# Kernel tuning notes

Hardware: AMD Instinct MI355X
Metric: run time of the kernel (lower is better)

The kernel has to match this reference:

```python
import jax, jax.numpy as jnp
import numpy as np
import math

B, T, C = 2, 2048, 1024
N_HEADS = 16  # config.head_size in the original (actually number of heads)
HEAD_DIM = C // N_HEADS


def setup_inputs() -> dict:
    key = jax.random.key(0)
    k1, k2, k3 = jax.random.split(key, 3)
    s = 1.0 / math.sqrt(C)
    return {
        "x": jax.random.normal(k1, (B, T, C), dtype=jnp.float32),
        "W_attn": jax.random.normal(k2, (C, 3 * C), dtype=jnp.float32) * s,
        "b_attn": jnp.zeros((3 * C,), dtype=jnp.float32),
        "W_proj": jax.random.normal(k3, (C, C), dtype=jnp.float32) * s,
        "b_proj": jnp.zeros((C,), dtype=jnp.float32),
    }


def reference(x, W_attn, b_attn, W_proj, b_proj):
    Bsz, Tlen, Cdim = x.shape
    qkv = x @ W_attn + b_attn                      # [B,T,3C]
    q, k, v = jnp.split(qkv, 3, axis=-1)
    # [B,T,C] -> [B,H,T,D]
    def to_heads(t):
        return t.reshape(Bsz, Tlen, N_HEADS, HEAD_DIM).transpose(0, 2, 1, 3)
    q, k, v = to_heads(q), to_heads(k), to_heads(v)
    # NOTE: original multiplies by sqrt(head_dim) (faithful to source, not 1/sqrt)
    scale = jnp.asarray(math.sqrt(HEAD_DIM), dtype=x.dtype)
    att = jnp.einsum("bhqd,bhkd->bhqk", q, k) * scale
    causal = jnp.tril(jnp.ones((Tlen, Tlen), dtype=bool))
    att = jnp.where(causal[None, None, :, :], att, jnp.asarray(-jnp.inf, x.dtype))
    att = jax.nn.softmax(att, axis=-1)
    # dropout layers are identity in eval mode
    y = jnp.einsum("bhqk,bhkd->bhqd", att, v)
    y = y.transpose(0, 2, 1, 3).reshape(Bsz, Tlen, Cdim)
    return y @ W_proj + b_proj
```

## Files before the change

kernel.cpp:

```cpp
#include <hip/hip_runtime.h>
#include <hip/hip_bf16.h>


#define B_  2
#define T_  2048
#define C_  1024
#define H_  16
#define D_  64
#define M_  (B_ * T_)
#define N3_ (3 * C_)

typedef __attribute__((ext_vector_type(8))) short s16x8;
typedef __attribute__((ext_vector_type(4))) short s16x4;
typedef __attribute__((ext_vector_type(4))) float f32x4;

typedef const __attribute__((address_space(1))) unsigned int gu32_t;
typedef __attribute__((address_space(3))) unsigned int lu32_t;

#define MFMA16(a, b, c) __builtin_amdgcn_mfma_f32_16x16x32_bf16(a, b, c, 0, 0, 0)

__device__ __forceinline__ void gload_lds16(const short* g, short* l) {
    __builtin_amdgcn_global_load_lds((gu32_t*)g, (lu32_t*)l, 16, 0, 0);
}

__device__ __forceinline__ float b2f(unsigned short u) {
    return __uint_as_float(((unsigned)u) << 16);
}
__device__ __forceinline__ unsigned short f2b(float f) {
    unsigned u = __float_as_uint(f);
    return (unsigned short)((u + 0x7FFFu + ((u >> 16) & 1u)) >> 16);
}
__device__ __forceinline__ float fexp2(float x) {
#if __has_builtin(__builtin_amdgcn_exp2f)
    return __builtin_amdgcn_exp2f(x);
#else
    return exp2f(x);
#endif
}

__global__ __launch_bounds__(256) void cvt_split(
    const float* __restrict__ in, short* __restrict__ oh, short* __restrict__ ol, int n)
{
    int i = (blockIdx.x * 256 + threadIdx.x) * 8;
    if (i >= n) return;
    float4 a = *(const float4*)&in[i];
    float4 b = *(const float4*)&in[i + 4];
    float v[8] = {a.x, a.y, a.z, a.w, b.x, b.y, b.z, b.w};
    s16x8 h, l;
    #pragma unroll
    for (int j = 0; j < 8; j++) {
        unsigned short hb = f2b(v[j]);
        h[j] = (short)hb;
        l[j] = (short)f2b(v[j] - b2f(hb));
    }
    *(s16x8*)&oh[i] = h;
    *(s16x8*)&ol[i] = l;
}

__global__ __launch_bounds__(256) void cvtT_split(
    const float* __restrict__ in, short* __restrict__ oh, short* __restrict__ ol,
    int R, int Cn)
{
    __shared__ short th[64][80];
    __shared__ short tl[64][80];
    const int tid = threadIdx.x;
    const int k0 = blockIdx.y * 64;
    const int n0 = blockIdx.x * 64;
    {
        int rl = tid >> 4, cl = (tid & 15) * 4;
        #pragma unroll
        for (int i = 0; i < 4; i++) {
            int kr = rl + i * 16;
            float4 v4 = *(const float4*)&in[(size_t)(k0 + kr) * Cn + n0 + cl];
            float v[4] = {v4.x, v4.y, v4.z, v4.w};
            #pragma unroll
            for (int j = 0; j < 4; j++) {
                unsigned short hb = f2b(v[j]);
                th[cl + j][kr] = (short)hb;
                tl[cl + j][kr] = (short)f2b(v[j] - b2f(hb));
            }
        }
    }
    __syncthreads();
    {
        int ro = tid >> 2, co = (tid & 3) * 16;
        *(s16x8*)&oh[(size_t)(n0 + ro) * R + k0 + co]     = *(s16x8*)&th[ro][co];
        *(s16x8*)&oh[(size_t)(n0 + ro) * R + k0 + co + 8] = *(s16x8*)&th[ro][co + 8];
        *(s16x8*)&ol[(size_t)(n0 + ro) * R + k0 + co]     = *(s16x8*)&tl[ro][co];
        *(s16x8*)&ol[(size_t)(n0 + ro) * R + k0 + co + 8] = *(s16x8*)&tl[ro][co + 8];
    }
}

__global__ __launch_bounds__(256) void cvtT_bf16(
    const float* __restrict__ in, short* __restrict__ out, int R, int Cn)
{
    __shared__ short t[64][80];
    const int tid = threadIdx.x;
    const int k0 = blockIdx.y * 64;
    const int n0 = blockIdx.x * 64;
    {
        int rl = tid >> 4, cl = (tid & 15) * 4;
        #pragma unroll
        for (int i = 0; i < 4; i++) {
            int kr = rl + i * 16;
            float4 v = *(const float4*)&in[(size_t)(k0 + kr) * Cn + n0 + cl];
            t[cl + 0][kr] = (short)f2b(v.x);
            t[cl + 1][kr] = (short)f2b(v.y);
            t[cl + 2][kr] = (short)f2b(v.z);
            t[cl + 3][kr] = (short)f2b(v.w);
        }
    }
    __syncthreads();
    {
        int ro = tid >> 2, co = (tid & 3) * 16;
        *(s16x8*)&out[(size_t)(n0 + ro) * R + k0 + co]     = *(s16x8*)&t[ro][co];
        *(s16x8*)&out[(size_t)(n0 + ro) * R + k0 + co + 8] = *(s16x8*)&t[ro][co + 8];
    }
}

__global__ __launch_bounds__(256) void qkv_qk(
    const short* __restrict__ Ah, const short* __restrict__ Al,
    const short* __restrict__ BTh, const short* __restrict__ BTl,
    const float* __restrict__ bias,
    short* __restrict__ Qh, short* __restrict__ Ql,
    short* __restrict__ Kh, short* __restrict__ Kl)
{
    __shared__ short Ash[128 * 32], Asl[128 * 32];
    __shared__ short Bsh[128 * 32], Bsl[128 * 32];

    const int tid  = threadIdx.x;
    const int wave = tid >> 6, lane = tid & 63;
    const int wm = wave >> 1, wn = wave & 1;
    const int lm = lane & 15, lq = lane >> 4;
    const int m0 = blockIdx.y * 128, n0 = blockIdx.x * 128;
    const int gr  = (lane >> 2);
    const int gc  = (((lane & 3) ^ ((lane >> 3) & 3)) << 3);
    const int sg  = ((lq ^ ((lm >> 1) & 3)) << 3);

    f32x4 acc[4][4] = {};

    for (int k0 = 0; k0 < C_; k0 += 32) {
        __syncthreads();
        #pragma unroll
        for (int j = 0; j < 2; j++) {
            int s = wave * 2 + j;
            int row = s * 16 + gr;
            size_t ga = (size_t)(m0 + row) * C_ + k0 + gc;
            size_t gb = (size_t)(n0 + row) * C_ + k0 + gc;
            gload_lds16(&Ah[ga],  &Ash[s * 512]);
            gload_lds16(&Al[ga],  &Asl[s * 512]);
            gload_lds16(&BTh[gb], &Bsh[s * 512]);
            gload_lds16(&BTl[gb], &Bsl[s * 512]);
        }
        __syncthreads();

        s16x8 ah[4], al[4], bh[4], bl[4];
        #pragma unroll
        for (int mi = 0; mi < 4; mi++) {
            int r = wm * 64 + mi * 16 + lm;
            ah[mi] = *(const s16x8*)&Ash[r * 32 + sg];
            al[mi] = *(const s16x8*)&Asl[r * 32 + sg];
        }
        #pragma unroll
        for (int nj = 0; nj < 4; nj++) {
            int r = wn * 64 + nj * 16 + lm;
            bh[nj] = *(const s16x8*)&Bsh[r * 32 + sg];
            bl[nj] = *(const s16x8*)&Bsl[r * 32 + sg];
        }
        #pragma unroll
        for (int mi = 0; mi < 4; mi++)
            #pragma unroll
            for (int nj = 0; nj < 4; nj++) {
                acc[mi][nj] = MFMA16(ah[mi], bh[nj], acc[mi][nj]);
                acc[mi][nj] = MFMA16(ah[mi], bl[nj], acc[mi][nj]);
                acc[mi][nj] = MFMA16(al[mi], bh[nj], acc[mi][nj]);
            }
    }

    #pragma unroll
    for (int nj = 0; nj < 4; nj++) {
        int n = n0 + wn * 64 + nj * 16 + lm;
        float bv = bias[n];
        int isK = n >> 10;
        int c = n & (C_ - 1);
        int h = c >> 6, d = c & (D_ - 1);
        short* dh = isK ? Kh : Qh;
        short* dl = isK ? Kl : Ql;
        float scale = isK ? 1.0f : 11.541560327111708f;
        #pragma unroll
        for (int mi = 0; mi < 4; mi++) {
            #pragma unroll
            for (int r = 0; r < 4; r++) {
                int m  = m0 + wm * 64 + mi * 16 + lq * 4 + r;
                int bb = m >> 11, t = m & (T_ - 1);
                float v = (acc[mi][nj][r] + bv) * scale;
                size_t idx = (((size_t)bb * H_ + h) * T_ + t) * D_ + d;
                unsigned short hb = f2b(v);
                dh[idx] = (short)hb;
                dl[idx] = (short)f2b(v - b2f(hb));
            }
        }
    }
}

__global__ __launch_bounds__(256, 4) void qkv_v(
    const short* __restrict__ Ah, const short* __restrict__ BTh,
    const float* __restrict__ bias, short* __restrict__ VT)
{
    __shared__ short Ash[64 * 32];
    __shared__ short Bsh[128 * 32];

    const int tid  = threadIdx.x;
    const int wave = tid >> 6, lane = tid & 63;
    const int wm = wave >> 1, wn = wave & 1;
    const int lm = lane & 15, lq = lane >> 4;
    const int m0 = blockIdx.y * 64, n0 = blockIdx.x * 128;
    const int gr  = (lane >> 2);
    const int gc  = (((lane & 3) ^ ((lane >> 3) & 3)) << 3);
    const int sg  = ((lq ^ ((lm >> 1) & 3)) << 3);

    f32x4 acc[2][4] = {};

    for (int k0 = 0; k0 < C_; k0 += 32) {
        __syncthreads();
        {
            int rowA = wave * 16 + gr;
            gload_lds16(&Ah[(size_t)(m0 + rowA) * C_ + k0 + gc], &Ash[wave * 512]);
            #pragma unroll
            for (int j = 0; j < 2; j++) {
                int s = wave * 2 + j;
                int rowB = s * 16 + gr;
                gload_lds16(&BTh[(size_t)(n0 + rowB) * C_ + k0 + gc], &Bsh[s * 512]);
            }
        }
        __syncthreads();

        s16x8 af[2], bfr[4];
        #pragma unroll
        for (int mi = 0; mi < 2; mi++)
            af[mi] = *(const s16x8*)&Ash[(wm * 32 + mi * 16 + lm) * 32 + sg];
        #pragma unroll
        for (int nj = 0; nj < 4; nj++)
            bfr[nj] = *(const s16x8*)&Bsh[(wn * 64 + nj * 16 + lm) * 32 + sg];
        #pragma unroll
        for (int mi = 0; mi < 2; mi++)
            #pragma unroll
            for (int nj = 0; nj < 4; nj++)
                acc[mi][nj] = MFMA16(af[mi], bfr[nj], acc[mi][nj]);
    }

    #pragma unroll
    for (int nj = 0; nj < 4; nj++) {
        int n = n0 + wn * 64 + nj * 16 + lm;
        float bv = bias[n];
        int h = n >> 6, d = n & (D_ - 1);
        #pragma unroll
        for (int mi = 0; mi < 2; mi++) {
            #pragma unroll
            for (int r = 0; r < 4; r++) {
                int m  = m0 + wm * 32 + mi * 16 + lq * 4 + r;
                int bb = m >> 11, t = m & (T_ - 1);
                VT[(((size_t)bb * H_ + h) * D_ + d) * T_ + t] =
                    (short)f2b(acc[mi][nj][r] + bv);
            }
        }
    }
}

__global__ __launch_bounds__(256, 4) void proj_mfma(
    const short* __restrict__ Ah, const short* __restrict__ BTh,
    const float* __restrict__ bias, float* __restrict__ out)
{
    __shared__ short Ash[64 * 32];
    __shared__ short Bsh[128 * 32];

    const int tid  = threadIdx.x;
    const int wave = tid >> 6, lane = tid & 63;
    const int wm = wave >> 1, wn = wave & 1;
    const int lm = lane & 15, lq = lane >> 4;
    const int m0 = blockIdx.y * 64, n0 = blockIdx.x * 128;
    const int gr  = (lane >> 2);
    const int gc  = (((lane & 3) ^ ((lane >> 3) & 3)) << 3);
    const int sg  = ((lq ^ ((lm >> 1) & 3)) << 3);

    f32x4 acc[2][4] = {};

    for (int k0 = 0; k0 < C_; k0 += 32) {
        __syncthreads();
        {
            int rowA = wave * 16 + gr;
            gload_lds16(&Ah[(size_t)(m0 + rowA) * C_ + k0 + gc], &Ash[wave * 512]);
            #pragma unroll
            for (int j = 0; j < 2; j++) {
                int s = wave * 2 + j;
                int rowB = s * 16 + gr;
                gload_lds16(&BTh[(size_t)(n0 + rowB) * C_ + k0 + gc], &Bsh[s * 512]);
            }
        }
        __syncthreads();

        s16x8 af[2], bfr[4];
        #pragma unroll
        for (int mi = 0; mi < 2; mi++)
            af[mi] = *(const s16x8*)&Ash[(wm * 32 + mi * 16 + lm) * 32 + sg];
        #pragma unroll
        for (int nj = 0; nj < 4; nj++)
            bfr[nj] = *(const s16x8*)&Bsh[(wn * 64 + nj * 16 + lm) * 32 + sg];
        #pragma unroll
        for (int mi = 0; mi < 2; mi++)
            #pragma unroll
            for (int nj = 0; nj < 4; nj++)
                acc[mi][nj] = MFMA16(af[mi], bfr[nj], acc[mi][nj]);
    }

    #pragma unroll
    for (int nj = 0; nj < 4; nj++) {
        int n = n0 + wn * 64 + nj * 16 + lm;
        float bv = bias[n];
        #pragma unroll
        for (int mi = 0; mi < 2; mi++) {
            #pragma unroll
            for (int r = 0; r < 4; r++) {
                int m = m0 + wm * 32 + mi * 16 + lq * 4 + r;
                out[(size_t)m * C_ + n] = acc[mi][nj][r] + bv;
            }
        }
    }
}

__device__ __forceinline__ void online_sm(
    f32x4 S[4], float& mrow, float& lrow, f32x4 O[4], int quad)
{
    float v[16];
    #pragma unroll
    for (int t = 0; t < 4; t++)
        #pragma unroll
        for (int r = 0; r < 4; r++) v[t * 4 + r] = S[t][r];
    #pragma unroll
    for (int s = 8; s; s >>= 1)
        #pragma unroll
        for (int i = 0; i < s; i++) v[i] = fmaxf(v[i], v[i + s]);
    float rm = v[0];
    rm = fmaxf(rm, __shfl_xor(rm, 16, 64));
    rm = fmaxf(rm, __shfl_xor(rm, 32, 64));
    if (!__all(rm - mrow <= 8.f)) {
        float mnew  = fmaxf(mrow, rm);
        float alpha = fexp2(mrow - mnew);
        mrow = mnew;
        lrow *= alpha;
        float al[4];
        #pragma unroll
        for (int r = 0; r < 4; r++) al[r] = __shfl(alpha, quad * 4 + r, 64);
        #pragma unroll
        for (int t = 0; t < 4; t++)
            #pragma unroll
            for (int r = 0; r < 4; r++) O[t][r] *= al[r];
    }
    float sv[16];
    #pragma unroll
    for (int t = 0; t < 4; t++)
        #pragma unroll
        for (int r = 0; r < 4; r++) {
            float p = fexp2(S[t][r] - mrow);
            S[t][r] = p;
            sv[t * 4 + r] = p;
        }
    #pragma unroll
    for (int s = 8; s; s >>= 1)
        #pragma unroll
        for (int i = 0; i < s; i++) sv[i] += sv[i + s];
    float rs = sv[0];
    rs += __shfl_xor(rs, 16, 64);
    rs += __shfl_xor(rs, 32, 64);
    lrow += rs;
}

__global__ __launch_bounds__(256, 2) void attn_mfma(
    const short* __restrict__ Qh, const short* __restrict__ Ql,
    const short* __restrict__ Kh, const short* __restrict__ Kl,
    const short* __restrict__ VT, short* __restrict__ Yb)
{
    __shared__ short Ksh[64][64], Ksl[64][64];
    __shared__ short Vt [64][64];
    __shared__ short Ps [4][2][16][64];

    const int tid  = threadIdx.x;
    const int wave = tid >> 6, lane = tid & 63;
    const int lm   = lane & 15, quad = lane >> 4;
    const int swz  = (lm & 7) << 3;

    const int bid = blockIdx.x;
    const int xcd = bid & 7;
    const int r_  = bid >> 3;
    const int bhl = r_ & 3;
    const int u   = r_ >> 2;
    const int g_  = u >> 3, j_ = u & 7;
    const int j   = g_ ? (15 - j_) : j_;
    const int bh  = xcd * 4 + bhl;
    const int b   = bh >> 4, h = bh & (H_ - 1);
    const int qtA = j, qtB = 31 - j;
    const int q0A = qtA * 64, q0B = qtB * 64;
    const size_t base  = (size_t)bh * T_ * D_;
    const size_t vbase = (size_t)bh * D_ * T_;

    const int src = tid >> 3;
    const int sch = (tid & 7) * 8;
    const int wsw = sch ^ ((src & 7) << 3);

    s16x8 bqhA[2], bqlA[2], bqhB[2], bqlB[2];
    #pragma unroll
    for (int kc = 0; kc < 2; kc++) {
        size_t ga = base + (size_t)(q0A + wave * 16 + lm) * D_ + kc * 32 + quad * 8;
        size_t gb = base + (size_t)(q0B + wave * 16 + lm) * D_ + kc * 32 + quad * 8;
        bqhA[kc] = *(const s16x8*)&Qh[ga];
        bqlA[kc] = *(const s16x8*)&Ql[ga];
        bqhB[kc] = *(const s16x8*)&Qh[gb];
        bqlB[kc] = *(const s16x8*)&Ql[gb];
    }

    s16x8 pkh[2], pkl[2], pvt[2];
    #pragma unroll
    for (int i = 0; i < 2; i++) {
        int row = i * 32 + src;
        size_t gk = base + (size_t)row * D_ + sch;
        pkh[i] = *(const s16x8*)&Kh[gk];
        pkl[i] = *(const s16x8*)&Kl[gk];
        pvt[i] = *(const s16x8*)&VT[vbase + (size_t)row * T_ + sch];
    }

    float mA = -INFINITY, lA = 0.f;
    float mB = -INFINITY, lB = 0.f;
    f32x4 OA[4] = {}, OB[4] = {};

    for (int kt = 0; kt <= qtB; kt++) {
        __syncthreads();
        #pragma unroll
        for (int i = 0; i < 2; i++) {
            int row = i * 32 + src;
            *(s16x8*)&Ksh[row][wsw] = pkh[i];
            *(s16x8*)&Ksl[row][wsw] = pkl[i];
            *(s16x8*)&Vt [row][wsw] = pvt[i];
        }
        if (kt < qtB) {
            #pragma unroll
            for (int i = 0; i < 2; i++) {
                int row = i * 32 + src;
                size_t gk = base + (size_t)((kt + 1) * 64 + row) * D_ + sch;
                pkh[i] = *(const s16x8*)&Kh[gk];
                pkl[i] = *(const s16x8*)&Kl[gk];
                pvt[i] = *(const s16x8*)&VT[vbase + (size_t)row * T_ + (kt + 1) * 64 + sch];
            }
        }
        __syncthreads();

        const bool doA = (kt <= qtA);
        const int  qg  = wave * 16 + lm;

        f32x4 SB[4] = {}, SA[4] = {};
        if (doA) {
            #pragma unroll
            for (int t = 0; t < 4; t++)
                #pragma unroll
                for (int kc = 0; kc < 2; kc++) {
                    s16x8 kh8 = *(const s16x8*)&Ksh[t * 16 + lm][(kc * 32 + quad * 8) ^ swz];
                    s16x8 kl8 = *(const s16x8*)&Ksl[t * 16 + lm][(kc * 32 + quad * 8) ^ swz];
                    SB[t] = MFMA16(kh8, bqhB[kc], SB[t]);
                    SB[t] = MFMA16(kl8, bqhB[kc], SB[t]);
                    SB[t] = MFMA16(kh8, bqlB[kc], SB[t]);
                    SA[t] = MFMA16(kh8, bqhA[kc], SA[t]);
                    SA[t] = MFMA16(kl8, bqhA[kc], SA[t]);
                    SA[t] = MFMA16(kh8, bqlA[kc], SA[t]);
                }
        } else {
            #pragma unroll
            for (int t = 0; t < 4; t++)
                #pragma unroll
                for (int kc = 0; kc < 2; kc++) {
                    s16x8 kh8 = *(const s16x8*)&Ksh[t * 16 + lm][(kc * 32 + quad * 8) ^ swz];
                    s16x8 kl8 = *(const s16x8*)&Ksl[t * 16 + lm][(kc * 32 + quad * 8) ^ swz];
                    SB[t] = MFMA16(kh8, bqhB[kc], SB[t]);
                    SB[t] = MFMA16(kl8, bqhB[kc], SB[t]);
                    SB[t] = MFMA16(kh8, bqlB[kc], SB[t]);
                }
        }

        if (kt == qtB) {
            #pragma unroll
            for (int t = 0; t < 4; t++)
                #pragma unroll
                for (int r = 0; r < 4; r++)
                    if ((t * 16 + quad * 4 + r) > qg) SB[t][r] = -INFINITY;
        }
        if (kt == qtA) {
            #pragma unroll
            for (int t = 0; t < 4; t++)
                #pragma unroll
                for (int r = 0; r < 4; r++)
                    if ((t * 16 + quad * 4 + r) > qg) SA[t][r] = -INFINITY;
        }

        online_sm(SB, mB, lB, OB, quad);
        if (doA) online_sm(SA, mA, lA, OA, quad);

        #pragma unroll
        for (int t = 0; t < 4; t++) {
            s16x4 p;
            #pragma unroll
            for (int r = 0; r < 4; r++)
                p[r] = (short)(__float_as_uint(SB[t][r]) >> 16);
            *(s16x4*)&Ps[wave][0][lm][(t * 16 + quad * 4) ^ swz] = p;
        }
        if (doA) {
            #pragma unroll
            for (int t = 0; t < 4; t++) {
                s16x4 p;
                #pragma unroll
                for (int r = 0; r < 4; r++)
                    p[r] = (short)(__float_as_uint(SA[t][r]) >> 16);
                *(s16x4*)&Ps[wave][1][lm][(t * 16 + quad * 4) ^ swz] = p;
            }
        }

        s16x8 apB[2], apA[2];
        #pragma unroll
        for (int kc = 0; kc < 2; kc++)
            apB[kc] = *(const s16x8*)&Ps[wave][0][lm][(kc * 32 + quad * 8) ^ swz];
        if (doA) {
            #pragma unroll
            for (int kc = 0; kc < 2; kc++)
                apA[kc] = *(const s16x8*)&Ps[wave][1][lm][(kc * 32 + quad * 8) ^ swz];
            #pragma unroll
            for (int t = 0; t < 4; t++)
                #pragma unroll
                for (int kc = 0; kc < 2; kc++) {
                    s16x8 bv = *(const s16x8*)&Vt[t * 16 + lm][(kc * 32 + quad * 8) ^ swz];
                    OB[t] = MFMA16(apB[kc], bv, OB[t]);
                    OA[t] = MFMA16(apA[kc], bv, OA[t]);
                }
        } else {
            #pragma unroll
            for (int t = 0; t < 4; t++)
                #pragma unroll
                for (int kc = 0; kc < 2; kc++) {
                    s16x8 bv = *(const s16x8*)&Vt[t * 16 + lm][(kc * 32 + quad * 8) ^ swz];
                    OB[t] = MFMA16(apB[kc], bv, OB[t]);
                }
        }
    }

    float liA[4], liB[4];
    #pragma unroll
    for (int r = 0; r < 4; r++) {
        liA[r] = 1.0f / __shfl(lA, quad * 4 + r, 64);
        liB[r] = 1.0f / __shfl(lB, quad * 4 + r, 64);
    }
    #pragma unroll
    for (int t = 0; t < 4; t++)
        #pragma unroll
        for (int r = 0; r < 4; r++) {
            int d  = t * 16 + lm;
            int qa = q0A + wave * 16 + quad * 4 + r;
            int qb = q0B + wave * 16 + quad * 4 + r;
            Yb[((size_t)b * T_ + qa) * C_ + h * D_ + d] =
                (short)f2b(OA[t][r] * liA[r]);
            Yb[((size_t)b * T_ + qb) * C_ + h * D_ + d] =
                (short)f2b(OB[t][r] * liB[r]);
        }
}

extern "C" void kernel_launch(void* const* d_in, const int* in_sizes, int n_in,
                              void* d_out, int out_size, void* d_ws, size_t ws_size,
                              hipStream_t stream)
{
    const float* x      = (const float*)d_in[0];
    const float* W_attn = (const float*)d_in[1];
    const float* b_attn = (const float*)d_in[2];
    const float* W_proj = (const float*)d_in[3];
    const float* b_proj = (const float*)d_in[4];
    float* out = (float*)d_out;

    char* ws = (char*)d_ws;
    const size_t MB = 1024 * 1024;
    short* Qh   = (short*)(ws);
    short* Ql   = (short*)(ws +  8 * MB);
    short* Kh   = (short*)(ws + 16 * MB);
    short* Kl   = (short*)(ws + 24 * MB);
    short* xh   = (short*)(ws + 32 * MB);
    short* xl   = (short*)(ws + 40 * MB);
    short* WaTh = (short*)(ws + 48 * MB);
    short* WaTl = (short*)(ws + 54 * MB);
    short* WpT  = (short*)(ws + 60 * MB);
    short* VT   = (short*)(ws + 40 * MB);
    short* Yb   = (short*)(ws + 32 * MB);

    cvt_split <<<dim3(M_ * C_ / 2048), 256, 0, stream>>>(x, xh, xl, M_ * C_);
    cvtT_split<<<dim3(N3_ / 64, C_ / 64), 256, 0, stream>>>(W_attn, WaTh, WaTl, C_, N3_);
    cvtT_bf16 <<<dim3(C_ / 64, C_ / 64), 256, 0, stream>>>(W_proj, WpT, C_, C_);

    qkv_qk <<<dim3(16, 32), 256, 0, stream>>>(xh, xl, WaTh, WaTl, b_attn,
                                              Qh, Ql, Kh, Kl);
    qkv_v  <<<dim3(8, 64), 256, 0, stream>>>(xh, WaTh + (size_t)2048 * C_,
                                             b_attn + 2048, VT);
    attn_mfma<<<dim3(512), 256, 0, stream>>>(Qh, Ql, Kh, Kl, VT, Yb);
    proj_mfma<<<dim3(8, 64), 256, 0, stream>>>(Yb, WpT, b_proj, out);
}
```

Before: 241.6 us.

## Double-buffer LDS in GEMM kernels with async prefetch two stages ahead

The three GEMM kernels (qkv_qk, qkv_v, proj_mfma) now use two LDS buffers. Global-to-LDS loads are issued two k-steps ahead and gated by explicit vmcnt waits and raw s_barrier, so memory latency overlaps MFMA work. The attention kernel also swaps __syncthreads for a raw barrier plus an lgkmcnt wait. This doubles LDS use per block, which may lower occupancy. The hand-written waitcnt counts must match the number of loads issued, otherwise the pipeline can race.

```diff
diff --git a/kernel.cpp b/kernel.cpp
--- a/kernel.cpp
+++ b/kernel.cpp
@@ -118,6 +118,20 @@
     }
 }
 
+#define QK_STAGE(buf, kk) do {                                          \
+    _Pragma("unroll")                                                   \
+    for (int j = 0; j < 2; j++) {                                       \
+        int s = wave * 2 + j;                                           \
+        int row = s * 16 + gr;                                          \
+        size_t ga = (size_t)(m0 + row) * C_ + (kk) + gc;                \
+        size_t gb = (size_t)(n0 + row) * C_ + (kk) + gc;                \
+        gload_lds16(&Ah[ga],  &Ash[buf][s * 512]);                      \
+        gload_lds16(&Al[ga],  &Asl[buf][s * 512]);                      \
+        gload_lds16(&BTh[gb], &Bsh[buf][s * 512]);                      \
+        gload_lds16(&BTl[gb], &Bsl[buf][s * 512]);                      \
+    }                                                                   \
+} while (0)
+
 __global__ __launch_bounds__(256) void qkv_qk(
     const short* __restrict__ Ah, const short* __restrict__ Al,
     const short* __restrict__ BTh, const short* __restrict__ BTl,
@@ -125,8 +139,8 @@
     short* __restrict__ Qh, short* __restrict__ Ql,
     short* __restrict__ Kh, short* __restrict__ Kl)
 {
-    __shared__ short Ash[128 * 32], Asl[128 * 32];
-    __shared__ short Bsh[128 * 32], Bsl[128 * 32];
+    __shared__ short Ash[2][128 * 32], Asl[2][128 * 32];
+    __shared__ short Bsh[2][128 * 32], Bsl[2][128 * 32];
 
     const int tid  = threadIdx.x;
     const int wave = tid >> 6, lane = tid & 63;
@@ -139,33 +153,28 @@
 
     f32x4 acc[4][4] = {};
 
-    for (int k0 = 0; k0 < C_; k0 += 32) {
-        __syncthreads();
-        #pragma unroll
-        for (int j = 0; j < 2; j++) {
-            int s = wave * 2 + j;
-            int row = s * 16 + gr;
-            size_t ga = (size_t)(m0 + row) * C_ + k0 + gc;
-            size_t gb = (size_t)(n0 + row) * C_ + k0 + gc;
-            gload_lds16(&Ah[ga],  &Ash[s * 512]);
-            gload_lds16(&Al[ga],  &Asl[s * 512]);
-            gload_lds16(&BTh[gb], &Bsh[s * 512]);
-            gload_lds16(&BTl[gb], &Bsl[s * 512]);
-        }
-        __syncthreads();
+    QK_STAGE(0, 0);
+    QK_STAGE(1, 32);
+
+    for (int it = 0; it < 32; ++it) {
+        const int cur = it & 1;
+        if (it == 31) asm volatile("s_waitcnt vmcnt(0)" ::: "memory");
+        else          asm volatile("s_waitcnt vmcnt(8)" ::: "memory");
+        __builtin_amdgcn_s_barrier();
+        __builtin_amdgcn_sched_barrier(0);
 
         s16x8 ah[4], al[4], bh[4], bl[4];
         #pragma unroll
         for (int mi = 0; mi < 4; mi++) {
             int r = wm * 64 + mi * 16 + lm;
-            ah[mi] = *(const s16x8*)&Ash[r * 32 + sg];
-            al[mi] = *(const s16x8*)&Asl[r * 32 + sg];
+            ah[mi] = *(const s16x8*)&Ash[cur][r * 32 + sg];
+            al[mi] = *(const s16x8*)&Asl[cur][r * 32 + sg];
         }
         #pragma unroll
         for (int nj = 0; nj < 4; nj++) {
             int r = wn * 64 + nj * 16 + lm;
-            bh[nj] = *(const s16x8*)&Bsh[r * 32 + sg];
-            bl[nj] = *(const s16x8*)&Bsl[r * 32 + sg];
+            bh[nj] = *(const s16x8*)&Bsh[cur][r * 32 + sg];
+            bl[nj] = *(const s16x8*)&Bsl[cur][r * 32 + sg];
         }
         #pragma unroll
         for (int mi = 0; mi < 4; mi++)
@@ -175,6 +184,10 @@
                 acc[mi][nj] = MFMA16(ah[mi], bl[nj], acc[mi][nj]);
                 acc[mi][nj] = MFMA16(al[mi], bh[nj], acc[mi][nj]);
             }
+
+        __builtin_amdgcn_sched_barrier(0);
+        __builtin_amdgcn_s_barrier();
+        if (it < 30) QK_STAGE(cur, (it + 2) * 32);
     }
 
     #pragma unroll
@@ -203,12 +216,27 @@
     }
 }
 
+#define V_STAGE(buf, kk) do {                                           \
+    {                                                                   \
+        int rowA = wave * 16 + gr;                                      \
+        gload_lds16(&Ah[(size_t)(m0 + rowA) * C_ + (kk) + gc],          \
+                    &Ash[buf][wave * 512]);                             \
+        _Pragma("unroll")                                               \
+        for (int j = 0; j < 2; j++) {                                   \
+            int s = wave * 2 + j;                                       \
+            int rowB = s * 16 + gr;                                     \
+            gload_lds16(&BTh[(size_t)(n0 + rowB) * C_ + (kk) + gc],     \
+                        &Bsh[buf][s * 512]);                            \
+        }                                                               \
+    }                                                                   \
+} while (0)
+
 __global__ __launch_bounds__(256, 4) void qkv_v(
     const short* __restrict__ Ah, const short* __restrict__ BTh,
     const float* __restrict__ bias, short* __restrict__ VT)
 {
-    __shared__ short Ash[64 * 32];
-    __shared__ short Bsh[128 * 32];
+    __shared__ short Ash[2][64 * 32];
+    __shared__ short Bsh[2][128 * 32];
 
     const int tid  = threadIdx.x;
     const int wave = tid >> 6, lane = tid & 63;
@@ -221,32 +249,32 @@
 
     f32x4 acc[2][4] = {};
 
-    for (int k0 = 0; k0 < C_; k0 += 32) {
-        __syncthreads();
-        {
-            int rowA = wave * 16 + gr;
-            gload_lds16(&Ah[(size_t)(m0 + rowA) * C_ + k0 + gc], &Ash[wave * 512]);
-            #pragma unroll
-            for (int j = 0; j < 2; j++) {
-                int s = wave * 2 + j;
-                int rowB = s * 16 + gr;
-                gload_lds16(&BTh[(size_t)(n0 + rowB) * C_ + k0 + gc], &Bsh[s * 512]);
-            }
-        }
-        __syncthreads();
+    V_STAGE(0, 0);
+    V_STAGE(1, 32);
+
+    for (int it = 0; it < 32; ++it) {
+        const int cur = it & 1;
+        if (it == 31) asm volatile("s_waitcnt vmcnt(0)" ::: "memory");
+        else          asm volatile("s_waitcnt vmcnt(3)" ::: "memory");
+        __builtin_amdgcn_s_barrier();
+        __builtin_amdgcn_sched_barrier(0);
 
         s16x8 af[2], bfr[4];
         #pragma unroll
         for (int mi = 0; mi < 2; mi++)
-            af[mi] = *(const s16x8*)&Ash[(wm * 32 + mi * 16 + lm) * 32 + sg];
+            af[mi] = *(const s16x8*)&Ash[cur][(wm * 32 + mi * 16 + lm) * 32 + sg];
         #pragma unroll
         for (int nj = 0; nj < 4; nj++)
-            bfr[nj] = *(const s16x8*)&Bsh[(wn * 64 + nj * 16 + lm) * 32 + sg];
+            bfr[nj] = *(const s16x8*)&Bsh[cur][(wn * 64 + nj * 16 + lm) * 32 + sg];
         #pragma unroll
         for (int mi = 0; mi < 2; mi++)
             #pragma unroll
             for (int nj = 0; nj < 4; nj++)
                 acc[mi][nj] = MFMA16(af[mi], bfr[nj], acc[mi][nj]);
+
+        __builtin_amdgcn_sched_barrier(0);
+        __builtin_amdgcn_s_barrier();
+        if (it < 30) V_STAGE(cur, (it + 2) * 32);
     }
 
     #pragma unroll
@@ -271,8 +299,8 @@
     const short* __restrict__ Ah, const short* __restrict__ BTh,
     const float* __restrict__ bias, float* __restrict__ out)
 {
-    __shared__ short Ash[64 * 32];
-    __shared__ short Bsh[128 * 32];
+    __shared__ short Ash[2][64 * 32];
+    __shared__ short Bsh[2][128 * 32];
 
     const int tid  = threadIdx.x;
     const int wave = tid >> 6, lane = tid & 63;
@@ -285,32 +313,32 @@
 
     f32x4 acc[2][4] = {};
 
-    for (int k0 = 0; k0 < C_; k0 += 32) {
-        __syncthreads();
-        {
-            int rowA = wave * 16 + gr;
-            gload_lds16(&Ah[(size_t)(m0 + rowA) * C_ + k0 + gc], &Ash[wave * 512]);
-            #pragma unroll
-            for (int j = 0; j < 2; j++) {
-                int s = wave * 2 + j;
-                int rowB = s * 16 + gr;
-                gload_lds16(&BTh[(size_t)(n0 + rowB) * C_ + k0 + gc], &Bsh[s * 512]);
-            }
-        }
-        __syncthreads();
+    V_STAGE(0, 0);
+    V_STAGE(1, 32);
+
+    for (int it = 0; it < 32; ++it) {
+        const int cur = it & 1;
+        if (it == 31) asm volatile("s_waitcnt vmcnt(0)" ::: "memory");
+        else          asm volatile("s_waitcnt vmcnt(3)" ::: "memory");
+        __builtin_amdgcn_s_barrier();
+        __builtin_amdgcn_sched_barrier(0);
 
         s16x8 af[2], bfr[4];
         #pragma unroll
         for (int mi = 0; mi < 2; mi++)
-            af[mi] = *(const s16x8*)&Ash[(wm * 32 + mi * 16 + lm) * 32 + sg];
+            af[mi] = *(const s16x8*)&Ash[cur][(wm * 32 + mi * 16 + lm) * 32 + sg];
         #pragma unroll
         for (int nj = 0; nj < 4; nj++)
-            bfr[nj] = *(const s16x8*)&Bsh[(wn * 64 + nj * 16 + lm) * 32 + sg];
+            bfr[nj] = *(const s16x8*)&Bsh[cur][(wn * 64 + nj * 16 + lm) * 32 + sg];
         #pragma unroll
         for (int mi = 0; mi < 2; mi++)
             #pragma unroll
             for (int nj = 0; nj < 4; nj++)
                 acc[mi][nj] = MFMA16(af[mi], bfr[nj], acc[mi][nj]);
+
+        __builtin_amdgcn_sched_barrier(0);
+        __builtin_amdgcn_s_barrier();
+        if (it < 30) V_STAGE(cur, (it + 2) * 32);
     }
 
     #pragma unroll
@@ -433,7 +461,7 @@
     f32x4 OA[4] = {}, OB[4] = {};
 
     for (int kt = 0; kt <= qtB; kt++) {
-        __syncthreads();
+        __builtin_amdgcn_s_barrier();
         #pragma unroll
         for (int i = 0; i < 2; i++) {
             int row = i * 32 + src;
@@ -451,7 +479,9 @@
                 pvt[i] = *(const s16x8*)&VT[vbase + (size_t)row * T_ + (kt + 1) * 64 + sch];
             }
         }
-        __syncthreads();
+        asm volatile("s_waitcnt lgkmcnt(0)" ::: "memory");
+        __builtin_amdgcn_s_barrier();
+        __builtin_amdgcn_sched_barrier(0);
 
         const bool doA = (kt <= qtA);
         const int  qg  = wave * 16 + lm;
```

After: 242.3 us. No clear change (+0.3%).

## Split causal attention into balanced KV halves with separate combine kernel

Applied to the files above, without the earlier changes.

Replaces the paired-query-tile attention kernel with a split-KV version. Each of 1024 blocks processes 16 or 17 KV steps. One group finishes the short query tile and then starts the long tile's remaining KV range, while the other group covers the long tile's first 17 KV tiles. Partial outputs and their max/sum statistics go to workspace, and a new combine kernel merges the two halves. The aim is to double the block count, raise occupancy (launch bound 4) and cut the MFMA work per step, adding priority hints. The cost is an extra launch, extra partial-output traffic, and rounding the partial outputs to bf16 before the merge.

```diff
diff --git a/kernel.cpp b/kernel.cpp
--- a/kernel.cpp
+++ b/kernel.cpp
@@ -375,14 +375,16 @@
     lrow += rs;
 }
 
-__global__ __launch_bounds__(256, 2) void attn_mfma(
+__global__ __launch_bounds__(256, 4) void attn_split(
     const short* __restrict__ Qh, const short* __restrict__ Ql,
     const short* __restrict__ Kh, const short* __restrict__ Kl,
-    const short* __restrict__ VT, short* __restrict__ Yb)
+    const short* __restrict__ VT, short* __restrict__ Yb,
+    short* __restrict__ PO0, short* __restrict__ PO1,
+    float* __restrict__ ML0, float* __restrict__ ML1)
 {
     __shared__ short Ksh[64][64], Ksl[64][64];
     __shared__ short Vt [64][64];
-    __shared__ short Ps [4][2][16][64];
+    __shared__ short Ps [4][16][64];
 
     const int tid  = threadIdx.x;
     const int wave = tid >> 6, lane = tid & 63;
@@ -394,28 +396,29 @@
     const int r_  = bid >> 3;
     const int bhl = r_ & 3;
     const int u   = r_ >> 2;
-    const int g_  = u >> 3, j_ = u & 7;
-    const int j   = g_ ? (15 - j_) : j_;
+    const int grp = u & 1;
+    const int j   = u >> 1;
     const int bh  = xcd * 4 + bhl;
     const int b   = bh >> 4, h = bh & (H_ - 1);
     const int qtA = j, qtB = 31 - j;
     const int q0A = qtA * 64, q0B = qtB * 64;
     const size_t base  = (size_t)bh * T_ * D_;
     const size_t vbase = (size_t)bh * D_ * T_;
+    const int pI = (bh << 4) | j;
 
     const int src = tid >> 3;
     const int sch = (tid & 7) * 8;
     const int wsw = sch ^ ((src & 7) << 3);
 
-    s16x8 bqhA[2], bqlA[2], bqhB[2], bqlB[2];
+    const int nsteps = (grp == 0) ? 17 : 16;
+
+    int q0 = grp ? q0A : q0B;
+    s16x8 bqh[2], bql[2];
     #pragma unroll
     for (int kc = 0; kc < 2; kc++) {
-        size_t ga = base + (size_t)(q0A + wave * 16 + lm) * D_ + kc * 32 + quad * 8;
-        size_t gb = base + (size_t)(q0B + wave * 16 + lm) * D_ + kc * 32 + quad * 8;
-        bqhA[kc] = *(const s16x8*)&Qh[ga];
-        bqlA[kc] = *(const s16x8*)&Ql[ga];
-        bqhB[kc] = *(const s16x8*)&Qh[gb];
-        bqlB[kc] = *(const s16x8*)&Ql[gb];
+        size_t gq = base + (size_t)(q0 + wave * 16 + lm) * D_ + kc * 32 + quad * 8;
+        bqh[kc] = *(const s16x8*)&Qh[gq];
+        bql[kc] = *(const s16x8*)&Ql[gq];
     }
 
     s16x8 pkh[2], pkl[2], pvt[2];
@@ -428,12 +431,11 @@
         pvt[i] = *(const s16x8*)&VT[vbase + (size_t)row * T_ + sch];
     }
 
-    float mA = -INFINITY, lA = 0.f;
-    float mB = -INFINITY, lB = 0.f;
-    f32x4 OA[4] = {}, OB[4] = {};
-
-    for (int kt = 0; kt <= qtB; kt++) {
-        __syncthreads();
+    float mrow = -INFINITY, lrow = 0.f;
+    f32x4 O[4] = {};
+
+    for (int step = 0; step < nsteps; ++step) {
+        __builtin_amdgcn_s_barrier();
         #pragma unroll
         for (int i = 0; i < 2; i++) {
             int row = i * 32 + src;
@@ -441,131 +443,150 @@
             *(s16x8*)&Ksl[row][wsw] = pkl[i];
             *(s16x8*)&Vt [row][wsw] = pvt[i];
         }
-        if (kt < qtB) {
+        if (step + 1 < nsteps) {
+            int sn  = step + 1;
+            int ktn = sn + ((grp && sn > j) ? (16 - j) : 0);
             #pragma unroll
             for (int i = 0; i < 2; i++) {
                 int row = i * 32 + src;
-                size_t gk = base + (size_t)((kt + 1) * 64 + row) * D_ + sch;
+                size_t gk = base + (size_t)(ktn * 64 + row) * D_ + sch;
                 pkh[i] = *(const s16x8*)&Kh[gk];
                 pkl[i] = *(const s16x8*)&Kl[gk];
-                pvt[i] = *(const s16x8*)&VT[vbase + (size_t)row * T_ + (kt + 1) * 64 + sch];
-            }
-        }
-        __syncthreads();
-
-        const bool doA = (kt <= qtA);
-        const int  qg  = wave * 16 + lm;
-
-        f32x4 SB[4] = {}, SA[4] = {};
-        if (doA) {
-            #pragma unroll
-            for (int t = 0; t < 4; t++)
-                #pragma unroll
-                for (int kc = 0; kc < 2; kc++) {
-                    s16x8 kh8 = *(const s16x8*)&Ksh[t * 16 + lm][(kc * 32 + quad * 8) ^ swz];
-                    s16x8 kl8 = *(const s16x8*)&Ksl[t * 16 + lm][(kc * 32 + quad * 8) ^ swz];
-                    SB[t] = MFMA16(kh8, bqhB[kc], SB[t]);
-                    SB[t] = MFMA16(kl8, bqhB[kc], SB[t]);
-                    SB[t] = MFMA16(kh8, bqlB[kc], SB[t]);
-                    SA[t] = MFMA16(kh8, bqhA[kc], SA[t]);
-                    SA[t] = MFMA16(kl8, bqhA[kc], SA[t]);
-                    SA[t] = MFMA16(kh8, bqlA[kc], SA[t]);
-                }
-        } else {
-            #pragma unroll
-            for (int t = 0; t < 4; t++)
-                #pragma unroll
-                for (int kc = 0; kc < 2; kc++) {
-                    s16x8 kh8 = *(const s16x8*)&Ksh[t * 16 + lm][(kc * 32 + quad * 8) ^ swz];
-                    s16x8 kl8 = *(const s16x8*)&Ksl[t * 16 + lm][(kc * 32 + quad * 8) ^ swz];
-                    SB[t] = MFMA16(kh8, bqhB[kc], SB[t]);
-                    SB[t] = MFMA16(kl8, bqhB[kc], SB[t]);
-                    SB[t] = MFMA16(kh8, bqlB[kc], SB[t]);
-                }
-        }
-
-        if (kt == qtB) {
+                pvt[i] = *(const s16x8*)&VT[vbase + (size_t)row * T_ + ktn * 64 + sch];
+            }
+        }
+        asm volatile("s_waitcnt lgkmcnt(0)" ::: "memory");
+        __builtin_amdgcn_s_barrier();
+        __builtin_amdgcn_sched_barrier(0);
+
+        const int kt    = step + ((grp && step > j) ? (16 - j) : 0);
+        const bool isA  = (grp == 1) && (step <= j);
+        const int curQt = isA ? qtA : qtB;
+        const int qg    = wave * 16 + lm;
+
+        f32x4 S[4] = {};
+        __builtin_amdgcn_s_setprio(1);
+        #pragma unroll
+        for (int t = 0; t < 4; t++)
+            #pragma unroll
+            for (int kc = 0; kc < 2; kc++) {
+                s16x8 kh8 = *(const s16x8*)&Ksh[t * 16 + lm][(kc * 32 + quad * 8) ^ swz];
+                s16x8 kl8 = *(const s16x8*)&Ksl[t * 16 + lm][(kc * 32 + quad * 8) ^ swz];
+                S[t] = MFMA16(kh8, bqh[kc], S[t]);
+                S[t] = MFMA16(kl8, bqh[kc], S[t]);
+                S[t] = MFMA16(kh8, bql[kc], S[t]);
+            }
+        __builtin_amdgcn_s_setprio(0);
+
+        if (kt == curQt) {
             #pragma unroll
             for (int t = 0; t < 4; t++)
                 #pragma unroll
                 for (int r = 0; r < 4; r++)
-                    if ((t * 16 + quad * 4 + r) > qg) SB[t][r] = -INFINITY;
-        }
-        if (kt == qtA) {
+                    if ((t * 16 + quad * 4 + r) > qg) S[t][r] = -INFINITY;
+        }
+
+        online_sm(S, mrow, lrow, O, quad);
+
+        #pragma unroll
+        for (int t = 0; t < 4; t++) {
+            s16x4 p;
+            #pragma unroll
+            for (int r = 0; r < 4; r++)
+                p[r] = (short)(__float_as_uint(S[t][r]) >> 16);
+            *(s16x4*)&Ps[wave][lm][(t * 16 + quad * 4) ^ swz] = p;
+        }
+
+        s16x8 ap[2];
+        #pragma unroll
+        for (int kc = 0; kc < 2; kc++)
+            ap[kc] = *(const s16x8*)&Ps[wave][lm][(kc * 32 + quad * 8) ^ swz];
+        __builtin_amdgcn_s_setprio(1);
+        #pragma unroll
+        for (int t = 0; t < 4; t++)
+            #pragma unroll
+            for (int kc = 0; kc < 2; kc++) {
+                s16x8 bv = *(const s16x8*)&Vt[t * 16 + lm][(kc * 32 + quad * 8) ^ swz];
+                O[t] = MFMA16(ap[kc], bv, O[t]);
+            }
+        __builtin_amdgcn_s_setprio(0);
+
+        if (grp == 1 && step == j) {
+            float li[4];
+            #pragma unroll
+            for (int r = 0; r < 4; r++)
+                li[r] = 1.0f / __shfl(lrow, quad * 4 + r, 64);
             #pragma unroll
             for (int t = 0; t < 4; t++)
                 #pragma unroll
-                for (int r = 0; r < 4; r++)
-                    if ((t * 16 + quad * 4 + r) > qg) SA[t][r] = -INFINITY;
-        }
-
-        online_sm(SB, mB, lB, OB, quad);
-        if (doA) online_sm(SA, mA, lA, OA, quad);
-
-        #pragma unroll
-        for (int t = 0; t < 4; t++) {
-            s16x4 p;
-            #pragma unroll
-            for (int r = 0; r < 4; r++)
-                p[r] = (short)(__float_as_uint(SB[t][r]) >> 16);
-            *(s16x4*)&Ps[wave][0][lm][(t * 16 + quad * 4) ^ swz] = p;
-        }
-        if (doA) {
-            #pragma unroll
-            for (int t = 0; t < 4; t++) {
-                s16x4 p;
-                #pragma unroll
-                for (int r = 0; r < 4; r++)
-                    p[r] = (short)(__float_as_uint(SA[t][r]) >> 16);
-                *(s16x4*)&Ps[wave][1][lm][(t * 16 + quad * 4) ^ swz] = p;
-            }
-        }
-
-        s16x8 apB[2], apA[2];
-        #pragma unroll
-        for (int kc = 0; kc < 2; kc++)
-            apB[kc] = *(const s16x8*)&Ps[wave][0][lm][(kc * 32 + quad * 8) ^ swz];
-        if (doA) {
-            #pragma unroll
-            for (int kc = 0; kc < 2; kc++)
-                apA[kc] = *(const s16x8*)&Ps[wave][1][lm][(kc * 32 + quad * 8) ^ swz];
+                for (int r = 0; r < 4; r++) {
+                    int q = q0A + wave * 16 + quad * 4 + r;
+                    Yb[((size_t)b * T_ + q) * C_ + h * D_ + t * 16 + lm] =
+                        (short)f2b(O[t][r] * li[r]);
+                }
+            mrow = -INFINITY; lrow = 0.f;
             #pragma unroll
             for (int t = 0; t < 4; t++)
                 #pragma unroll
-                for (int kc = 0; kc < 2; kc++) {
-                    s16x8 bv = *(const s16x8*)&Vt[t * 16 + lm][(kc * 32 + quad * 8) ^ swz];
-                    OB[t] = MFMA16(apB[kc], bv, OB[t]);
-                    OA[t] = MFMA16(apA[kc], bv, OA[t]);
-                }
-        } else {
-            #pragma unroll
-            for (int t = 0; t < 4; t++)
-                #pragma unroll
-                for (int kc = 0; kc < 2; kc++) {
-                    s16x8 bv = *(const s16x8*)&Vt[t * 16 + lm][(kc * 32 + quad * 8) ^ swz];
-                    OB[t] = MFMA16(apB[kc], bv, OB[t]);
-                }
-        }
-    }
-
-    float liA[4], liB[4];
-    #pragma unroll
-    for (int r = 0; r < 4; r++) {
-        liA[r] = 1.0f / __shfl(lA, quad * 4 + r, 64);
-        liB[r] = 1.0f / __shfl(lB, quad * 4 + r, 64);
+                for (int r = 0; r < 4; r++) O[t][r] = 0.f;
+            #pragma unroll
+            for (int kc = 0; kc < 2; kc++) {
+                size_t gq = base + (size_t)(q0B + wave * 16 + lm) * D_ + kc * 32 + quad * 8;
+                bqh[kc] = *(const s16x8*)&Qh[gq];
+                bql[kc] = *(const s16x8*)&Ql[gq];
+            }
+        }
+    }
+
+    short* POd = grp ? PO1 : PO0;
+    float* MLd = grp ? ML1 : ML0;
+    if (quad == 0) {
+        MLd[pI * 128 + (wave * 16 + lm) * 2 + 0] = mrow;
+        MLd[pI * 128 + (wave * 16 + lm) * 2 + 1] = lrow;
     }
     #pragma unroll
     for (int t = 0; t < 4; t++)
         #pragma unroll
         for (int r = 0; r < 4; r++) {
-            int d  = t * 16 + lm;
-            int qa = q0A + wave * 16 + quad * 4 + r;
-            int qb = q0B + wave * 16 + quad * 4 + r;
-            Yb[((size_t)b * T_ + qa) * C_ + h * D_ + d] =
-                (short)f2b(OA[t][r] * liA[r]);
-            Yb[((size_t)b * T_ + qb) * C_ + h * D_ + d] =
-                (short)f2b(OB[t][r] * liB[r]);
-        }
+            int rr = wave * 16 + quad * 4 + r;
+            POd[((size_t)pI * 64 + rr) * 64 + t * 16 + lm] = (short)f2b(O[t][r]);
+        }
+}
+
+__global__ __launch_bounds__(256) void attn_combine(
+    const short* __restrict__ PO0, const short* __restrict__ PO1,
+    const float* __restrict__ ML0, const float* __restrict__ ML1,
+    short* __restrict__ Yb)
+{
+    const int p  = blockIdx.x;
+    const int bh = p >> 4, j = p & 15;
+    const int b  = bh >> 4, h = bh & (H_ - 1);
+    const int q0B = (31 - j) * 64;
+    const int t  = threadIdx.x;
+    const int r  = t >> 2, cs = (t & 3) * 16;
+
+    float m0 = ML0[p * 128 + r * 2 + 0], l0 = ML0[p * 128 + r * 2 + 1];
+    float m1 = ML1[p * 128 + r * 2 + 0], l1 = ML1[p * 128 + r * 2 + 1];
+    float mC = fmaxf(m0, m1);
+    float a0 = fexp2(m0 - mC), a1 = fexp2(m1 - mC);
+    float li = 1.0f / (a0 * l0 + a1 * l1);
+
+    const short* p0 = &PO0[((size_t)p * 64 + r) * 64 + cs];
+    const short* p1 = &PO1[((size_t)p * 64 + r) * 64 + cs];
+    short* y = &Yb[((size_t)b * T_ + q0B + r) * C_ + h * D_ + cs];
+    #pragma unroll
+    for (int s = 0; s < 2; s++) {
+        s16x8 o0 = *(const s16x8*)&p0[s * 8];
+        s16x8 o1 = *(const s16x8*)&p1[s * 8];
+        s16x8 o;
+        #pragma unroll
+        for (int e = 0; e < 8; e++) {
+            float f = (b2f((unsigned short)o0[e]) * a0 +
+                       b2f((unsigned short)o1[e]) * a1) * li;
+            o[e] = (short)f2b(f);
+        }
+        *(s16x8*)&y[s * 8] = o;
+    }
 }
 
 extern "C" void kernel_launch(void* const* d_in, const int* in_sizes, int n_in,
@@ -592,6 +613,10 @@
     short* WpT  = (short*)(ws + 60 * MB);
     short* VT   = (short*)(ws + 40 * MB);
     short* Yb   = (short*)(ws + 32 * MB);
+    short* PO0  = (short*)(ws + 48 * MB);
+    short* PO1  = (short*)(ws + 52 * MB);
+    float* ML0  = (float*)(ws + 56 * MB);
+    float* ML1  = (float*)(ws + 56 * MB + 512 * 1024);
 
     cvt_split <<<dim3(M_ * C_ / 2048), 256, 0, stream>>>(x, xh, xl, M_ * C_);
     cvtT_split<<<dim3(N3_ / 64, C_ / 64), 256, 0, stream>>>(W_attn, WaTh, WaTl, C_, N3_);
@@ -601,6 +626,8 @@
                                               Qh, Ql, Kh, Kl);
     qkv_v  <<<dim3(8, 64), 256, 0, stream>>>(xh, WaTh + (size_t)2048 * C_,
                                              b_attn + 2048, VT);
-    attn_mfma<<<dim3(512), 256, 0, stream>>>(Qh, Ql, Kh, Kl, VT, Yb);
+    attn_split  <<<dim3(1024), 256, 0, stream>>>(Qh, Ql, Kh, Kl, VT, Yb,
+                                                 PO0, PO1, ML0, ML1);
+    attn_combine<<<dim3(512), 256, 0, stream>>>(PO0, PO1, ML0, ML1, Yb);
     proj_mfma<<<dim3(8, 64), 256, 0, stream>>>(Yb, WpT, b_proj, out);
 }
```

New measurement: 246.3 us. Within noise of the previous version (+1.9%).
